# Kernel optimization log

Hardware: AMD Instinct MI355X
Metric: run time of the kernel (lower is better)

The kernel has to match this reference:

```python
import jax, jax.numpy as jnp
import numpy as np
import math

HEAD_DIM = 128
THETA = 10000.0
MASK_VAL = -10000.0


def _rope(x, cos, sin):
    # x: (B, S, D); cos/sin: (S, D//2). Pairs (even, odd) rotated as complex.
    xr = x.reshape(*x.shape[:-1], -1, 2)
    xe, xo = xr[..., 0], xr[..., 1]
    oe = xe * cos - xo * sin
    oo = xe * sin + xo * cos
    return jnp.stack([oe, oo], axis=-1).reshape(x.shape)


def setup_inputs() -> dict:
    key = jax.random.key(0)
    B, S, D = 8, 4096, HEAD_DIM
    qkv = jax.random.normal(key, (B, S, 3 * D), dtype=jnp.float32)
    return {"qkv": qkv}


def reference(qkv):
    B, S, threeD = qkv.shape
    D = threeD // 3
    qkv = qkv.reshape(B, S, 3, D)
    q, k, v = qkv[:, :, 0], qkv[:, :, 1], qkv[:, :, 2]

    # precompute_freqs_cis: outer(t, 1/theta^(2i/d)) -> cos/sin (S, D//2)
    inv_freq = 1.0 / (THETA ** (jnp.arange(0, D, 2, dtype=jnp.float32) / D))
    freqs = jnp.arange(S, dtype=jnp.float32)[:, None] * inv_freq[None, :]
    cos, sin = jnp.cos(freqs), jnp.sin(freqs)
    q = _rope(q, cos, sin)
    k = _rope(k, cos, sin)

    scale = 1.0 / math.sqrt(D)
    scores = jnp.einsum('btd,bsd->bts', q, k) * scale  # (B, S, S)
    causal_mask = jnp.triu(jnp.full((S, S), MASK_VAL, dtype=scores.dtype), 1)
    attn = jax.nn.softmax(scores + causal_mask, axis=-1)
    out = jnp.einsum('bts,bsd->btd', attn, v)  # (B, S, D)
    return out
```

## Files before the change

### kernel.cpp

```cpp
#include <hip/hip_runtime.h>
#include <math.h>

typedef _Float16 half8 __attribute__((ext_vector_type(8)));
typedef float floatx4 __attribute__((ext_vector_type(4)));
typedef float floatx2 __attribute__((ext_vector_type(2)));

#define B_ 8
#define S_ 4096
#define SCALE_L2E 0.12751743008389106f
#define MASK_L2E  -14426.950408889634f
#define L2_10K_OVER_128 0.10381025296522975f

#define PLD2 40
#define KW  136
#define VW  24
#define OSTLD 136
#define SLOTS_PER_B 576
#define NW 8
#define KVBUF 8192
#define NBUF 3
#define POFF (NBUF * KVBUF)
#define POOL_HALFS (POFF + NW * 2 * 16 * PLD2)

__device__ __forceinline__ int chunk_prefix(int qt32) {
    int g = qt32 >> 4;
    return qt32 + 8 * g * (g - 1) + (qt32 - (g << 4)) * g;
}

__device__ __forceinline__ void glds16(const _Float16* src, _Float16* dst) {
    __builtin_amdgcn_global_load_lds((const __attribute__((address_space(1))) void*)src,
                                     (__attribute__((address_space(3))) void*)dst, 16, 0, 0);
}

__global__ __launch_bounds__(256) void prep_kernel(const float* __restrict__ qkv,
                                                   _Float16* __restrict__ Qh,
                                                   _Float16* __restrict__ Kp,
                                                   _Float16* __restrict__ Vp) {
    __shared__ __align__(16) _Float16 Kl[16][KW];
    __shared__ __align__(16) _Float16 Vt[128][VW];
    const int tid = threadIdx.x;
    const int b   = blockIdx.y;
    const int s0  = blockIdx.x * 16;

#pragma unroll
    for (int it = 0; it < 4; ++it) {
        int idx = tid + it * 256;
        int i = idx & 63, sr = idx >> 6, s = s0 + sr;
        const float* base = qkv + ((size_t)(b * S_ + s)) * 384 + 2 * i;
        floatx2 q2 = *(const floatx2*)base;
        floatx2 k2 = *(const floatx2*)(base + 128);
        float inv = exp2f(-(float)(2 * i) * L2_10K_OVER_128);
        float ang = (float)s * inv;
        float sn, cs;
        __sincosf(ang, &sn, &cs);
        size_t oq = ((size_t)(b * S_ + s)) * 128 + 2 * i;
        Qh[oq]     = (_Float16)((q2[0] * cs - q2[1] * sn) * SCALE_L2E);
        Qh[oq + 1] = (_Float16)((q2[0] * sn + q2[1] * cs) * SCALE_L2E);
        Kl[sr][2 * i]     = (_Float16)(k2[0] * cs - k2[1] * sn);
        Kl[sr][2 * i + 1] = (_Float16)(k2[0] * sn + k2[1] * cs);
    }
#pragma unroll
    for (int it = 0; it < 2; ++it) {
        int idx = tid + it * 256;
        int c = idx & 31, sr = idx >> 5;
        floatx4 v = *(const floatx4*)(qkv + ((size_t)(b * S_ + s0 + sr)) * 384 + 256 + c * 4);
#pragma unroll
        for (int j = 0; j < 4; ++j) Vt[c * 4 + j][sr] = (_Float16)v[j];
    }
    __syncthreads();

    {
        int c = tid >> 6, lane = tid & 63;
        int quad = lane >> 4, n = lane & 15;
        half8 val = *(const half8*)&Kl[n][c * 32 + quad * 8];
        int s16 = s0 >> 4;
        *(half8*)(Kp + (((size_t)(b * 256 + s16) * 4 + c) * 64 + lane) * 8) = val;
    }
    {
        int kt = s0 >> 6, c2 = (s0 >> 5) & 1, qp = (s0 >> 4) & 1;
        int nt = tid >> 5, lq = (tid >> 4) & 1, n = tid & 15;
        int quad = qp * 2 + lq;
        int lane = quad * 16 + n;
        half8 val = *(const half8*)&Vt[nt * 16 + n][lq * 8];
        *(half8*)(Vp + ((((size_t)(b * 64 + kt) * 2 + c2) * 8 + nt) * 64 + lane) * 8) = val;
    }
}

__global__ __launch_bounds__(512) void attn_part_kernel(const _Float16* __restrict__ Qh,
                                                        const _Float16* __restrict__ Kp,
                                                        const _Float16* __restrict__ Vp,
                                                        _Float16* __restrict__ Ppart,
                                                        float* __restrict__ Lpart) {
    __shared__ __align__(16) _Float16 POOL[POOL_HALFS];

    const int tid  = threadIdx.x;
    const int w    = tid >> 6;
    const int lane = tid & 63;
    const int quad = lane >> 4;
    const int l16  = lane & 15;
    const int b     = blockIdx.x & 7;
    const int chunk = blockIdx.x >> 3;
    const int c0    = chunk * 8;

    const int qt32_top  = 127 - blockIdx.y * 8;
    const int ktmax_blk = (qt32_top * 32 + 31) >> 6;
    if (c0 > ktmax_blk) return;
    const int kend_blk  = min(ktmax_blk, c0 + 7);

    const int qt32   = qt32_top - w;
    const int qr0    = qt32 * 32;
    const int kt_max = (qr0 + 31) >> 6;
    const bool has_work = (c0 <= kt_max);
    const int kend   = min(kt_max, c0 + 7);
    const int slot   = b * SLOTS_PER_B + chunk_prefix(qt32) + chunk;
    _Float16* Pw = POOL + POFF + w * (2 * 16 * PLD2);

    half8 aq[2][4];
#pragma unroll
    for (int tile = 0; tile < 2; ++tile) {
        const _Float16* Qb = Qh + ((size_t)(b * S_) + qr0 + tile * 16 + l16) * 128;
#pragma unroll
        for (int c = 0; c < 4; ++c) aq[tile][c] = *(const half8*)(Qb + c * 32 + quad * 8);
    }

    floatx4 o[2][8];
#pragma unroll
    for (int tile = 0; tile < 2; ++tile)
#pragma unroll
        for (int i = 0; i < 8; ++i) o[tile][i] = (floatx4){0.f, 0.f, 0.f, 0.f};
    float rsum[2][4] = {{0.f, 0.f, 0.f, 0.f}, {0.f, 0.f, 0.f, 0.f}};

    const _Float16* Kb = Kp + (size_t)b * 524288;
    const _Float16* Vb = Vp + (size_t)b * 524288;

    const int ht0    = 2 * c0;
    const int ht_end = 2 * kend_blk + 1;

#define STAGE(ht_)                                                                \
    do {                                                                          \
        const _Float16* ks_ = Kb + (size_t)(ht_) * 4096 + w * 512 + lane * 8;     \
        const _Float16* vs_ = Vb + (size_t)(ht_) * 4096 + w * 512 + lane * 8;     \
        _Float16* d_ = POOL + ((ht_) % NBUF) * KVBUF + w * 512;                   \
        glds16(ks_, d_);                                                          \
        glds16(vs_, d_ + 4096);                                                   \
    } while (0)

    STAGE(ht0);
    STAGE(ht0 + 1);

    for (int ht = ht0; ht <= ht_end; ++ht) {
        if (ht < ht_end) {
            asm volatile("s_waitcnt vmcnt(2)" ::: "memory");
        } else {
            asm volatile("s_waitcnt vmcnt(0)" ::: "memory");
        }
        __builtin_amdgcn_s_barrier();
        if (ht + 2 <= ht_end) STAGE(ht + 2);

        const int kt = ht >> 1, h = ht & 1;
        if (has_work && kt <= kend) {
            const _Float16* Klds = POOL + (ht % NBUF) * KVBUF;
            const _Float16* Vlds = Klds + 4096;

            floatx4 s4[2][2];
#pragma unroll
            for (int tl = 0; tl < 2; ++tl) {
                half8 bk[4];
#pragma unroll
                for (int c = 0; c < 4; ++c)
                    bk[c] = *(const half8*)&Klds[((tl * 4 + c) * 64 + lane) * 8];
                floatx4 a0 = (floatx4){0.f, 0.f, 0.f, 0.f};
                floatx4 a1 = (floatx4){0.f, 0.f, 0.f, 0.f};
#pragma unroll
                for (int c = 0; c < 4; ++c) {
                    a0 = __builtin_amdgcn_mfma_f32_16x16x32_f16(aq[0][c], bk[c], a0, 0, 0, 0);
                    a1 = __builtin_amdgcn_mfma_f32_16x16x32_f16(aq[1][c], bk[c], a1, 0, 0, 0);
                }
                s4[0][tl] = a0; s4[1][tl] = a1;
            }

            half8 vf[8];
#pragma unroll
            for (int nt = 0; nt < 8; ++nt)
                vf[nt] = *(const half8*)&Vlds[(nt * 64 + lane) * 8];

            if (kt == kt_max) {
#pragma unroll
                for (int tile = 0; tile < 2; ++tile)
#pragma unroll
                    for (int tl = 0; tl < 2; ++tl)
#pragma unroll
                        for (int r = 0; r < 4; ++r) {
                            int kcol = kt * 64 + h * 32 + tl * 16 + l16;
                            int qr   = qr0 + tile * 16 + quad * 4 + r;
                            if (kcol > qr) s4[tile][tl][r] += MASK_L2E;
                        }
            }

#pragma unroll
            for (int tile = 0; tile < 2; ++tile)
#pragma unroll
                for (int tl = 0; tl < 2; ++tl)
#pragma unroll
                    for (int r = 0; r < 4; ++r) {
                        float p = __builtin_amdgcn_exp2f(s4[tile][tl][r]);
                        rsum[tile][r] += p;
                        Pw[tile * (16 * PLD2) + (quad * 4 + r) * PLD2 + tl * 16 + l16] = (_Float16)p;
                    }

#pragma unroll
            for (int tile = 0; tile < 2; ++tile) {
                half8 ap = *(const half8*)&Pw[tile * (16 * PLD2) + l16 * PLD2 + quad * 8];
#pragma unroll
                for (int nt = 0; nt < 8; ++nt)
                    o[tile][nt] = __builtin_amdgcn_mfma_f32_16x16x32_f16(ap, vf[nt], o[tile][nt], 0, 0, 0);
            }
        }
    }
#undef STAGE

    __builtin_amdgcn_s_barrier();

    if (!has_work) return;

#pragma unroll
    for (int off = 1; off <= 8; off <<= 1)
#pragma unroll
        for (int tile = 0; tile < 2; ++tile)
#pragma unroll
            for (int r = 0; r < 4; ++r)
                rsum[tile][r] += __shfl_xor(rsum[tile][r], off, 64);
    if (l16 == 0) {
#pragma unroll
        for (int tile = 0; tile < 2; ++tile)
#pragma unroll
            for (int r = 0; r < 4; ++r)
                Lpart[(size_t)slot * 32 + tile * 16 + quad * 4 + r] = rsum[tile][r];
    }

    _Float16* Ost = POOL + w * (POOL_HALFS / NW);
    _Float16* pp = Ppart + (size_t)slot * 4096;
#pragma unroll
    for (int tile = 0; tile < 2; ++tile) {
#pragma unroll
        for (int nt = 0; nt < 8; ++nt)
#pragma unroll
            for (int r = 0; r < 4; ++r)
                Ost[(quad * 4 + r) * OSTLD + nt * 16 + l16] = (_Float16)o[tile][nt][r];
#pragma unroll
        for (int i = 0; i < 4; ++i) {
            int idx = lane + i * 64;
            half8 v = *(const half8*)&Ost[(idx >> 4) * OSTLD + (idx & 15) * 8];
            *(half8*)(pp + ((size_t)tile * 256 + idx) * 8) = v;
        }
    }
}

__global__ __launch_bounds__(256) void reduce_kernel(const _Float16* __restrict__ Ppart,
                                                     const float* __restrict__ Lpart,
                                                     float* __restrict__ out) {
    const int bid  = blockIdx.x;
    const int b    = bid >> 7;
    const int qt32 = bid & 127;
    const int qr0  = qt32 * 32;
    const int nch  = (((qr0 + 31) >> 6) >> 3) + 1;
    const int slot0 = b * SLOTS_PER_B + chunk_prefix(qt32);
    const _Float16* pp = Ppart + (size_t)slot0 * 4096;
    const float* lp = Lpart + (size_t)slot0 * 32;
    const int tid = threadIdx.x;

#pragma unroll
    for (int j = 0; j < 2; ++j) {
        int idx = tid + j * 256;
        int row = idx >> 4;
        float acc[8] = {0.f, 0.f, 0.f, 0.f, 0.f, 0.f, 0.f, 0.f};
        float l = 0.f;
        for (int c = 0; c < nch; ++c) {
            half8 v = *(const half8*)(pp + (size_t)c * 4096 + (size_t)idx * 8);
#pragma unroll
            for (int k = 0; k < 8; ++k) acc[k] += (float)v[k];
            l += lp[c * 32 + row];
        }
        float inv = 1.0f / l;
        float* ob = out + ((size_t)(b * S_) + qr0) * 128 + (size_t)idx * 8;
        floatx4 o0 = (floatx4){acc[0] * inv, acc[1] * inv, acc[2] * inv, acc[3] * inv};
        floatx4 o1 = (floatx4){acc[4] * inv, acc[5] * inv, acc[6] * inv, acc[7] * inv};
        *(floatx4*)ob = o0;
        *(floatx4*)(ob + 4) = o1;
    }
}

#define PLD 72
__global__ __launch_bounds__(64) void attn_atomic_kernel(const _Float16* __restrict__ Qh,
                                                         const _Float16* __restrict__ Kp,
                                                         const _Float16* __restrict__ Vp,
                                                         float* __restrict__ out,
                                                         float* __restrict__ Lg) {
    __shared__ __align__(16) _Float16 Pl[2][16 * PLD];
    const int lane = threadIdx.x, quad = lane >> 4, l16 = lane & 15;
    const int b = blockIdx.x & 7, chunk = blockIdx.x >> 3;
    const int qt = 255 - blockIdx.y, qr0 = qt * 16;
    const int kt_max = qt >> 2, c0 = chunk * 8;
    if (c0 > kt_max) return;
    const int kend = min(kt_max, c0 + 7);
    const _Float16* Qb = Qh + ((size_t)(b * S_) + qr0 + l16) * 128;
    half8 aq[4];
#pragma unroll
    for (int c = 0; c < 4; ++c) aq[c] = *(const half8*)(Qb + c * 32 + quad * 8);
    floatx4 o[8];
#pragma unroll
    for (int i = 0; i < 8; ++i) o[i] = (floatx4){0.f, 0.f, 0.f, 0.f};
    float rsum[4] = {0.f, 0.f, 0.f, 0.f};
    const _Float16* Kb = Kp + (size_t)b * 524288;
    const _Float16* Vb = Vp + (size_t)b * 524288;
    for (int kt = c0; kt <= kend; ++kt) {
        half8 vf[2][8];
#pragma unroll
        for (int c2 = 0; c2 < 2; ++c2)
#pragma unroll
            for (int nt = 0; nt < 8; ++nt)
                vf[c2][nt] = *(const half8*)(Vb + (((size_t)(kt * 2 + c2) * 8 + nt) * 64 + lane) * 8);
        floatx4 s4[4];
#pragma unroll
        for (int t = 0; t < 4; ++t) {
            const _Float16* kp = Kb + ((size_t)((kt * 4 + t) * 4) * 64 + lane) * 8;
            floatx4 acc = (floatx4){0.f, 0.f, 0.f, 0.f};
#pragma unroll
            for (int c = 0; c < 4; ++c) {
                half8 bk = *(const half8*)(kp + c * 512);
                acc = __builtin_amdgcn_mfma_f32_16x16x32_f16(aq[c], bk, acc, 0, 0, 0);
            }
            s4[t] = acc;
        }
        if (kt == kt_max) {
#pragma unroll
            for (int t = 0; t < 4; ++t)
#pragma unroll
                for (int r = 0; r < 4; ++r) {
                    int kcol = kt * 64 + t * 16 + l16;
                    int qr = qr0 + quad * 4 + r;
                    if (kcol > qr) s4[t][r] += MASK_L2E;
                }
        }
        const int buf = kt & 1;
#pragma unroll
        for (int t = 0; t < 4; ++t)
#pragma unroll
            for (int r = 0; r < 4; ++r) {
                float p = __builtin_amdgcn_exp2f(s4[t][r]);
                rsum[r] += p;
                Pl[buf][(quad * 4 + r) * PLD + t * 16 + l16] = (_Float16)p;
            }
#pragma unroll
        for (int c2 = 0; c2 < 2; ++c2) {
            half8 ap = *(const half8*)&Pl[buf][l16 * PLD + c2 * 32 + quad * 8];
#pragma unroll
            for (int nt = 0; nt < 8; ++nt)
                o[nt] = __builtin_amdgcn_mfma_f32_16x16x32_f16(ap, vf[c2][nt], o[nt], 0, 0, 0);
        }
    }
#pragma unroll
    for (int off = 1; off <= 8; off <<= 1)
#pragma unroll
        for (int r = 0; r < 4; ++r)
            rsum[r] += __shfl_xor(rsum[r], off, 64);
    if (l16 == 0) {
#pragma unroll
        for (int r = 0; r < 4; ++r)
            atomicAdd(&Lg[(size_t)(b * S_) + qr0 + quad * 4 + r], rsum[r]);
    }
    float* ob = out + ((size_t)(b * S_) + qr0) * 128;
#pragma unroll
    for (int nt = 0; nt < 8; ++nt)
#pragma unroll
        for (int r = 0; r < 4; ++r)
            atomicAdd(&ob[(quad * 4 + r) * 128 + nt * 16 + l16], o[nt][r]);
}

__global__ __launch_bounds__(256) void norm_kernel(float* __restrict__ out,
                                                   const float* __restrict__ Lg) {
    int i = blockIdx.x * 256 + threadIdx.x;
    int row = i >> 5;
    floatx4 v = *(floatx4*)(out + (size_t)i * 4);
    float inv = 1.0f / Lg[row];
    v[0] *= inv; v[1] *= inv; v[2] *= inv; v[3] *= inv;
    *(floatx4*)(out + (size_t)i * 4) = v;
}

extern "C" void kernel_launch(void* const* d_in, const int* in_sizes, int n_in,
                              void* d_out, int out_size, void* d_ws, size_t ws_size,
                              hipStream_t stream) {
    const float* qkv = (const float*)d_in[0];
    float* out = (float*)d_out;
    const size_t MB = 1024 * 1024;
    _Float16* Qh = (_Float16*)d_ws;
    _Float16* Kp = (_Float16*)((char*)d_ws + 8 * MB);
    _Float16* Vp = (_Float16*)((char*)d_ws + 16 * MB);

    const size_t lpart_bytes = (size_t)B_ * SLOTS_PER_B * 32 * sizeof(float);
    const size_t ppart_bytes = (size_t)B_ * SLOTS_PER_B * 4096 * sizeof(_Float16);
    const size_t need = 25 * MB + ppart_bytes;

    prep_kernel<<<dim3(256, B_), dim3(256), 0, stream>>>(qkv, Qh, Kp, Vp);

    if (ws_size >= need) {
        float*    Lpart = (float*)((char*)d_ws + 24 * MB);
        _Float16* Ppart = (_Float16*)((char*)d_ws + 25 * MB);
        (void)lpart_bytes;
        attn_part_kernel<<<dim3(64, 16), dim3(512), 0, stream>>>(Qh, Kp, Vp, Ppart, Lpart);
        reduce_kernel<<<dim3(1024), dim3(256), 0, stream>>>(Ppart, Lpart, out);
    } else {
        float* Lg = (float*)((char*)d_ws + 24 * MB);
        hipMemsetAsync(out, 0, (size_t)B_ * S_ * 128 * sizeof(float), stream);
        hipMemsetAsync(Lg, 0, (size_t)B_ * S_ * sizeof(float), stream);
        attn_atomic_kernel<<<dim3(64, 256), dim3(64), 0, stream>>>(Qh, Kp, Vp, out, Lg);
        norm_kernel<<<dim3(4096), dim3(256), 0, stream>>>(out, Lg);
    }
}
```

Baseline: 165.0 us.

## Compute transposed scores so P stays in registers via lane shuffles, drop LDS P staging

The QK^T MFMA operands are swapped so each lane holds scores for one query row across four key columns. The exponentiated probabilities are then packed to fp16 and rearranged with cross-lane shuffles into the A-operand layout for the PV MFMA, which removes the per-wave LDS round trip for P and the extra LDS space. Row sums become one scalar per tile and need fewer shuffles at the end. The grid dimensions are also swapped, which changes the order in which blocks are dispatched.

```diff
diff --git a/kernel.cpp b/kernel.cpp
--- a/kernel.cpp
+++ b/kernel.cpp
@@ -11,7 +11,6 @@
 #define MASK_L2E  -14426.950408889634f
 #define L2_10K_OVER_128 0.10381025296522975f
 
-#define PLD2 40
 #define KW  136
 #define VW  24
 #define OSTLD 136
@@ -19,8 +18,7 @@
 #define NW 8
 #define KVBUF 8192
 #define NBUF 3
-#define POFF (NBUF * KVBUF)
-#define POOL_HALFS (POFF + NW * 2 * 16 * PLD2)
+#define POOL_HALFS (NBUF * KVBUF)
 
 __device__ __forceinline__ int chunk_prefix(int qt32) {
     int g = qt32 >> 4;
@@ -30,6 +28,12 @@
 __device__ __forceinline__ void glds16(const _Float16* src, _Float16* dst) {
     __builtin_amdgcn_global_load_lds((const __attribute__((address_space(1))) void*)src,
                                      (__attribute__((address_space(3))) void*)dst, 16, 0, 0);
+}
+
+__device__ __forceinline__ unsigned pack2(float a, float b) {
+    union { _Float16 h[2]; unsigned u; } x;
+    x.h[0] = (_Float16)a; x.h[1] = (_Float16)b;
+    return x.u;
 }
 
 __global__ __launch_bounds__(256) void prep_kernel(const float* __restrict__ qkv,
@@ -98,11 +102,11 @@
     const int lane = tid & 63;
     const int quad = lane >> 4;
     const int l16  = lane & 15;
-    const int b     = blockIdx.x & 7;
-    const int chunk = blockIdx.x >> 3;
+    const int b     = blockIdx.y & 7;
+    const int chunk = blockIdx.y >> 3;
     const int c0    = chunk * 8;
 
-    const int qt32_top  = 127 - blockIdx.y * 8;
+    const int qt32_top  = 127 - blockIdx.x * 8;
     const int ktmax_blk = (qt32_top * 32 + 31) >> 6;
     if (c0 > ktmax_blk) return;
     const int kend_blk  = min(ktmax_blk, c0 + 7);
@@ -113,7 +117,6 @@
     const bool has_work = (c0 <= kt_max);
     const int kend   = min(kt_max, c0 + 7);
     const int slot   = b * SLOTS_PER_B + chunk_prefix(qt32) + chunk;
-    _Float16* Pw = POOL + POFF + w * (2 * 16 * PLD2);
 
     half8 aq[2][4];
 #pragma unroll
@@ -128,7 +131,7 @@
     for (int tile = 0; tile < 2; ++tile)
 #pragma unroll
         for (int i = 0; i < 8; ++i) o[tile][i] = (floatx4){0.f, 0.f, 0.f, 0.f};
-    float rsum[2][4] = {{0.f, 0.f, 0.f, 0.f}, {0.f, 0.f, 0.f, 0.f}};
+    float rsum[2] = {0.f, 0.f};
 
     const _Float16* Kb = Kp + (size_t)b * 524288;
     const _Float16* Vb = Vp + (size_t)b * 524288;
@@ -162,21 +165,21 @@
             const _Float16* Klds = POOL + (ht % NBUF) * KVBUF;
             const _Float16* Vlds = Klds + 4096;
 
-            floatx4 s4[2][2];
-#pragma unroll
-            for (int tl = 0; tl < 2; ++tl) {
+            floatx4 st[2][2];
+#pragma unroll
+            for (int t = 0; t < 2; ++t) {
                 half8 bk[4];
 #pragma unroll
                 for (int c = 0; c < 4; ++c)
-                    bk[c] = *(const half8*)&Klds[((tl * 4 + c) * 64 + lane) * 8];
+                    bk[c] = *(const half8*)&Klds[((t * 4 + c) * 64 + lane) * 8];
                 floatx4 a0 = (floatx4){0.f, 0.f, 0.f, 0.f};
                 floatx4 a1 = (floatx4){0.f, 0.f, 0.f, 0.f};
 #pragma unroll
                 for (int c = 0; c < 4; ++c) {
-                    a0 = __builtin_amdgcn_mfma_f32_16x16x32_f16(aq[0][c], bk[c], a0, 0, 0, 0);
-                    a1 = __builtin_amdgcn_mfma_f32_16x16x32_f16(aq[1][c], bk[c], a1, 0, 0, 0);
+                    a0 = __builtin_amdgcn_mfma_f32_16x16x32_f16(bk[c], aq[0][c], a0, 0, 0, 0);
+                    a1 = __builtin_amdgcn_mfma_f32_16x16x32_f16(bk[c], aq[1][c], a1, 0, 0, 0);
                 }
-                s4[0][tl] = a0; s4[1][tl] = a1;
+                st[0][t] = a0; st[1][t] = a1;
             }
 
             half8 vf[8];
@@ -188,32 +191,47 @@
 #pragma unroll
                 for (int tile = 0; tile < 2; ++tile)
 #pragma unroll
-                    for (int tl = 0; tl < 2; ++tl)
+                    for (int t = 0; t < 2; ++t)
 #pragma unroll
                         for (int r = 0; r < 4; ++r) {
-                            int kcol = kt * 64 + h * 32 + tl * 16 + l16;
-                            int qr   = qr0 + tile * 16 + quad * 4 + r;
-                            if (kcol > qr) s4[tile][tl][r] += MASK_L2E;
+                            int kcol = kt * 64 + h * 32 + t * 16 + quad * 4 + r;
+                            int qr   = qr0 + tile * 16 + l16;
+                            if (kcol > qr) st[tile][t][r] += MASK_L2E;
                         }
             }
 
 #pragma unroll
-            for (int tile = 0; tile < 2; ++tile)
-#pragma unroll
-                for (int tl = 0; tl < 2; ++tl)
-#pragma unroll
-                    for (int r = 0; r < 4; ++r) {
-                        float p = __builtin_amdgcn_exp2f(s4[tile][tl][r]);
-                        rsum[tile][r] += p;
-                        Pw[tile * (16 * PLD2) + (quad * 4 + r) * PLD2 + tl * 16 + l16] = (_Float16)p;
-                    }
-
-#pragma unroll
             for (int tile = 0; tile < 2; ++tile) {
-                half8 ap = *(const half8*)&Pw[tile * (16 * PLD2) + l16 * PLD2 + quad * 8];
+                float e00 = __builtin_amdgcn_exp2f(st[tile][0][0]);
+                float e01 = __builtin_amdgcn_exp2f(st[tile][0][1]);
+                float e02 = __builtin_amdgcn_exp2f(st[tile][0][2]);
+                float e03 = __builtin_amdgcn_exp2f(st[tile][0][3]);
+                float e10 = __builtin_amdgcn_exp2f(st[tile][1][0]);
+                float e11 = __builtin_amdgcn_exp2f(st[tile][1][1]);
+                float e12 = __builtin_amdgcn_exp2f(st[tile][1][2]);
+                float e13 = __builtin_amdgcn_exp2f(st[tile][1][3]);
+                rsum[tile] += ((e00 + e01) + (e02 + e03)) + ((e10 + e11) + (e12 + e13));
+                unsigned p0a = pack2(e00, e01), p0b = pack2(e02, e03);
+                unsigned p1a = pack2(e10, e11), p1b = pack2(e12, e13);
+                const int base = ((quad & 1) << 5) + l16;
+                unsigned q0a = (unsigned)__shfl((int)p0a, base);
+                unsigned q0b = (unsigned)__shfl((int)p0b, base);
+                unsigned q0c = (unsigned)__shfl((int)p0a, base + 16);
+                unsigned q0d = (unsigned)__shfl((int)p0b, base + 16);
+                unsigned q1a = (unsigned)__shfl((int)p1a, base);
+                unsigned q1b = (unsigned)__shfl((int)p1b, base);
+                unsigned q1c = (unsigned)__shfl((int)p1a, base + 16);
+                unsigned q1d = (unsigned)__shfl((int)p1b, base + 16);
+                const bool hi = (quad & 2) != 0;
+                union { unsigned u[4]; half8 v; } pk;
+                pk.u[0] = hi ? q1a : q0a;
+                pk.u[1] = hi ? q1b : q0b;
+                pk.u[2] = hi ? q1c : q0c;
+                pk.u[3] = hi ? q1d : q0d;
+                half8 pa = pk.v;
 #pragma unroll
                 for (int nt = 0; nt < 8; ++nt)
-                    o[tile][nt] = __builtin_amdgcn_mfma_f32_16x16x32_f16(ap, vf[nt], o[tile][nt], 0, 0, 0);
+                    o[tile][nt] = __builtin_amdgcn_mfma_f32_16x16x32_f16(pa, vf[nt], o[tile][nt], 0, 0, 0);
             }
         }
     }
@@ -224,18 +242,14 @@
     if (!has_work) return;
 
 #pragma unroll
-    for (int off = 1; off <= 8; off <<= 1)
+    for (int tile = 0; tile < 2; ++tile) {
+        rsum[tile] += __shfl_xor(rsum[tile], 16, 64);
+        rsum[tile] += __shfl_xor(rsum[tile], 32, 64);
+    }
+    if (quad == 0) {
 #pragma unroll
         for (int tile = 0; tile < 2; ++tile)
-#pragma unroll
-            for (int r = 0; r < 4; ++r)
-                rsum[tile][r] += __shfl_xor(rsum[tile][r], off, 64);
-    if (l16 == 0) {
-#pragma unroll
-        for (int tile = 0; tile < 2; ++tile)
-#pragma unroll
-            for (int r = 0; r < 4; ++r)
-                Lpart[(size_t)slot * 32 + tile * 16 + quad * 4 + r] = rsum[tile][r];
+            Lpart[(size_t)slot * 32 + tile * 16 + l16] = rsum[tile];
     }
 
     _Float16* Ost = POOL + w * (POOL_HALFS / NW);
@@ -407,7 +421,7 @@
         float*    Lpart = (float*)((char*)d_ws + 24 * MB);
         _Float16* Ppart = (_Float16*)((char*)d_ws + 25 * MB);
         (void)lpart_bytes;
-        attn_part_kernel<<<dim3(64, 16), dim3(512), 0, stream>>>(Qh, Kp, Vp, Ppart, Lpart);
+        attn_part_kernel<<<dim3(16, 64), dim3(512), 0, stream>>>(Qh, Kp, Vp, Ppart, Lpart);
         reduce_kernel<<<dim3(1024), dim3(256), 0, stream>>>(Ppart, Lpart, out);
     } else {
         float* Lg = (float*)((char*)d_ws + 24 * MB);
```

Measured after the change: 183.7 us. +11.3%, slower.

## Give each wave 64 query rows and compact the split-K grid to active blocks

Applied to the files above, without the earlier changes.

Each wave now owns a 64-row query tile (four 16-row MFMA tiles) instead of 32 rows, and each block has 4 waves instead of 8. Every K/V fragment loaded from LDS is therefore reused across twice as many query rows. The grid enumerates only blocks that have work instead of launching blocks that exit early. The costs are much higher register pressure from 4x8 accumulators, fewer waves per block for latency hiding, and a different partial-buffer layout in the reduction.

```diff
diff --git a/kernel.cpp b/kernel.cpp
--- a/kernel.cpp
+++ b/kernel.cpp
@@ -15,16 +15,16 @@
 #define KW  136
 #define VW  24
 #define OSTLD 136
-#define SLOTS_PER_B 576
-#define NW 8
+#define SLOTS64_PER_B 288
+#define NW 4
 #define KVBUF 8192
 #define NBUF 3
 #define POFF (NBUF * KVBUF)
-#define POOL_HALFS (POFF + NW * 2 * 16 * PLD2)
-
-__device__ __forceinline__ int chunk_prefix(int qt32) {
-    int g = qt32 >> 4;
-    return qt32 + 8 * g * (g - 1) + (qt32 - (g << 4)) * g;
+#define POOL_HALFS (POFF + NW * 16 * PLD2)
+
+__device__ __forceinline__ int chunk_prefix64(int i) {
+    int g = i >> 3;
+    return i + 4 * g * (g - 1) + (i - (g << 3)) * g;
 }
 
 __device__ __forceinline__ void glds16(const _Float16* src, _Float16* dst) {
@@ -86,7 +86,7 @@
     }
 }
 
-__global__ __launch_bounds__(512) void attn_part_kernel(const _Float16* __restrict__ Qh,
+__global__ __launch_bounds__(256) void attn_part_kernel(const _Float16* __restrict__ Qh,
                                                         const _Float16* __restrict__ Kp,
                                                         const _Float16* __restrict__ Vp,
                                                         _Float16* __restrict__ Ppart,
@@ -98,37 +98,41 @@
     const int lane = tid & 63;
     const int quad = lane >> 4;
     const int l16  = lane & 15;
-    const int b     = blockIdx.x & 7;
-    const int chunk = blockIdx.x >> 3;
+    const int b    = blockIdx.x;
+
+    int u = blockIdx.y, g = 0;
+    for (;;) { int c = ((63 - 4 * g) >> 3) + 1; if (u < c) break; u -= c; ++g; }
+    const int chunk = u;
     const int c0    = chunk * 8;
-
-    const int qt32_top  = 127 - blockIdx.y * 8;
-    const int ktmax_blk = (qt32_top * 32 + 31) >> 6;
-    if (c0 > ktmax_blk) return;
-    const int kend_blk  = min(ktmax_blk, c0 + 7);
-
-    const int qt32   = qt32_top - w;
-    const int qr0    = qt32 * 32;
-    const int kt_max = (qr0 + 31) >> 6;
+    const int i_top = 63 - 4 * g;
+    const int kend_blk = min(i_top, c0 + 7);
+
+    const int unit  = i_top - w;
+    const int qr0   = unit * 64;
+    const int kt_max = unit;
     const bool has_work = (c0 <= kt_max);
-    const int kend   = min(kt_max, c0 + 7);
-    const int slot   = b * SLOTS_PER_B + chunk_prefix(qt32) + chunk;
-    _Float16* Pw = POOL + POFF + w * (2 * 16 * PLD2);
-
-    half8 aq[2][4];
-#pragma unroll
-    for (int tile = 0; tile < 2; ++tile) {
+    const int kend  = min(kt_max, c0 + 7);
+    const int slot  = b * SLOTS64_PER_B + chunk_prefix64(unit) + chunk;
+    _Float16* Pw = POOL + POFF + w * (16 * PLD2);
+
+    half8 aq[4][4];
+#pragma unroll
+    for (int tile = 0; tile < 4; ++tile) {
         const _Float16* Qb = Qh + ((size_t)(b * S_) + qr0 + tile * 16 + l16) * 128;
 #pragma unroll
         for (int c = 0; c < 4; ++c) aq[tile][c] = *(const half8*)(Qb + c * 32 + quad * 8);
     }
 
-    floatx4 o[2][8];
-#pragma unroll
-    for (int tile = 0; tile < 2; ++tile)
+    floatx4 o[4][8];
+#pragma unroll
+    for (int tile = 0; tile < 4; ++tile)
 #pragma unroll
         for (int i = 0; i < 8; ++i) o[tile][i] = (floatx4){0.f, 0.f, 0.f, 0.f};
-    float rsum[2][4] = {{0.f, 0.f, 0.f, 0.f}, {0.f, 0.f, 0.f, 0.f}};
+    float rsum[4][4];
+#pragma unroll
+    for (int tile = 0; tile < 4; ++tile)
+#pragma unroll
+        for (int r = 0; r < 4; ++r) rsum[tile][r] = 0.f;
 
     const _Float16* Kb = Kp + (size_t)b * 524288;
     const _Float16* Vb = Vp + (size_t)b * 524288;
@@ -138,11 +142,13 @@
 
 #define STAGE(ht_)                                                                \
     do {                                                                          \
-        const _Float16* ks_ = Kb + (size_t)(ht_) * 4096 + w * 512 + lane * 8;     \
-        const _Float16* vs_ = Vb + (size_t)(ht_) * 4096 + w * 512 + lane * 8;     \
-        _Float16* d_ = POOL + ((ht_) % NBUF) * KVBUF + w * 512;                   \
+        const _Float16* ks_ = Kb + (size_t)(ht_) * 4096 + w * 1024 + lane * 8;    \
+        const _Float16* vs_ = Vb + (size_t)(ht_) * 4096 + w * 1024 + lane * 8;    \
+        _Float16* d_ = POOL + ((ht_) % NBUF) * KVBUF + w * 1024;                  \
         glds16(ks_, d_);                                                          \
+        glds16(ks_ + 512, d_ + 512);                                              \
         glds16(vs_, d_ + 4096);                                                   \
+        glds16(vs_ + 512, d_ + 4096 + 512);                                       \
     } while (0)
 
     STAGE(ht0);
@@ -150,7 +156,7 @@
 
     for (int ht = ht0; ht <= ht_end; ++ht) {
         if (ht < ht_end) {
-            asm volatile("s_waitcnt vmcnt(2)" ::: "memory");
+            asm volatile("s_waitcnt vmcnt(4)" ::: "memory");
         } else {
             asm volatile("s_waitcnt vmcnt(0)" ::: "memory");
         }
@@ -162,55 +168,44 @@
             const _Float16* Klds = POOL + (ht % NBUF) * KVBUF;
             const _Float16* Vlds = Klds + 4096;
 
-            floatx4 s4[2][2];
-#pragma unroll
-            for (int tl = 0; tl < 2; ++tl) {
-                half8 bk[4];
+            half8 bk[2][4];
+#pragma unroll
+            for (int tl = 0; tl < 2; ++tl)
 #pragma unroll
                 for (int c = 0; c < 4; ++c)
-                    bk[c] = *(const half8*)&Klds[((tl * 4 + c) * 64 + lane) * 8];
-                floatx4 a0 = (floatx4){0.f, 0.f, 0.f, 0.f};
-                floatx4 a1 = (floatx4){0.f, 0.f, 0.f, 0.f};
-#pragma unroll
-                for (int c = 0; c < 4; ++c) {
-                    a0 = __builtin_amdgcn_mfma_f32_16x16x32_f16(aq[0][c], bk[c], a0, 0, 0, 0);
-                    a1 = __builtin_amdgcn_mfma_f32_16x16x32_f16(aq[1][c], bk[c], a1, 0, 0, 0);
-                }
-                s4[0][tl] = a0; s4[1][tl] = a1;
-            }
-
+                    bk[tl][c] = *(const half8*)&Klds[((tl * 4 + c) * 64 + lane) * 8];
             half8 vf[8];
 #pragma unroll
             for (int nt = 0; nt < 8; ++nt)
                 vf[nt] = *(const half8*)&Vlds[(nt * 64 + lane) * 8];
 
-            if (kt == kt_max) {
-#pragma unroll
-                for (int tile = 0; tile < 2; ++tile)
-#pragma unroll
-                    for (int tl = 0; tl < 2; ++tl)
-#pragma unroll
-                        for (int r = 0; r < 4; ++r) {
-                            int kcol = kt * 64 + h * 32 + tl * 16 + l16;
-                            int qr   = qr0 + tile * 16 + quad * 4 + r;
-                            if (kcol > qr) s4[tile][tl][r] += MASK_L2E;
-                        }
-            }
-
-#pragma unroll
-            for (int tile = 0; tile < 2; ++tile)
-#pragma unroll
-                for (int tl = 0; tl < 2; ++tl)
+#pragma unroll
+            for (int tile = 0; tile < 4; ++tile) {
+                floatx4 s0 = (floatx4){0.f, 0.f, 0.f, 0.f};
+                floatx4 s1 = (floatx4){0.f, 0.f, 0.f, 0.f};
+#pragma unroll
+                for (int c = 0; c < 4; ++c) {
+                    s0 = __builtin_amdgcn_mfma_f32_16x16x32_f16(aq[tile][c], bk[0][c], s0, 0, 0, 0);
+                    s1 = __builtin_amdgcn_mfma_f32_16x16x32_f16(aq[tile][c], bk[1][c], s1, 0, 0, 0);
+                }
+                if (kt == kt_max) {
 #pragma unroll
                     for (int r = 0; r < 4; ++r) {
-                        float p = __builtin_amdgcn_exp2f(s4[tile][tl][r]);
-                        rsum[tile][r] += p;
-                        Pw[tile * (16 * PLD2) + (quad * 4 + r) * PLD2 + tl * 16 + l16] = (_Float16)p;
+                        int qr = qr0 + tile * 16 + quad * 4 + r;
+                        int k0 = kt * 64 + h * 32 + l16;
+                        if (k0 > qr)      s0[r] += MASK_L2E;
+                        if (k0 + 16 > qr) s1[r] += MASK_L2E;
                     }
-
-#pragma unroll
-            for (int tile = 0; tile < 2; ++tile) {
-                half8 ap = *(const half8*)&Pw[tile * (16 * PLD2) + l16 * PLD2 + quad * 8];
+                }
+#pragma unroll
+                for (int r = 0; r < 4; ++r) {
+                    float p0 = __builtin_amdgcn_exp2f(s0[r]);
+                    float p1 = __builtin_amdgcn_exp2f(s1[r]);
+                    rsum[tile][r] += p0 + p1;
+                    Pw[(quad * 4 + r) * PLD2 + l16]      = (_Float16)p0;
+                    Pw[(quad * 4 + r) * PLD2 + 16 + l16] = (_Float16)p1;
+                }
+                half8 ap = *(const half8*)&Pw[l16 * PLD2 + quad * 8];
 #pragma unroll
                 for (int nt = 0; nt < 8; ++nt)
                     o[tile][nt] = __builtin_amdgcn_mfma_f32_16x16x32_f16(ap, vf[nt], o[tile][nt], 0, 0, 0);
@@ -226,22 +221,22 @@
 #pragma unroll
     for (int off = 1; off <= 8; off <<= 1)
 #pragma unroll
-        for (int tile = 0; tile < 2; ++tile)
+        for (int tile = 0; tile < 4; ++tile)
 #pragma unroll
             for (int r = 0; r < 4; ++r)
                 rsum[tile][r] += __shfl_xor(rsum[tile][r], off, 64);
     if (l16 == 0) {
 #pragma unroll
-        for (int tile = 0; tile < 2; ++tile)
+        for (int tile = 0; tile < 4; ++tile)
 #pragma unroll
             for (int r = 0; r < 4; ++r)
-                Lpart[(size_t)slot * 32 + tile * 16 + quad * 4 + r] = rsum[tile][r];
+                Lpart[(size_t)slot * 64 + tile * 16 + quad * 4 + r] = rsum[tile][r];
     }
 
     _Float16* Ost = POOL + w * (POOL_HALFS / NW);
-    _Float16* pp = Ppart + (size_t)slot * 4096;
-#pragma unroll
-    for (int tile = 0; tile < 2; ++tile) {
+    _Float16* pp = Ppart + (size_t)slot * 8192;
+#pragma unroll
+    for (int tile = 0; tile < 4; ++tile) {
 #pragma unroll
         for (int nt = 0; nt < 8; ++nt)
 #pragma unroll
@@ -251,7 +246,7 @@
         for (int i = 0; i < 4; ++i) {
             int idx = lane + i * 64;
             half8 v = *(const half8*)&Ost[(idx >> 4) * OSTLD + (idx & 15) * 8];
-            *(half8*)(pp + ((size_t)tile * 256 + idx) * 8) = v;
+            *(half8*)(pp + ((size_t)tile * 2048 + (size_t)idx * 8)) = v;
         }
     }
 }
@@ -260,26 +255,26 @@
                                                      const float* __restrict__ Lpart,
                                                      float* __restrict__ out) {
     const int bid  = blockIdx.x;
-    const int b    = bid >> 7;
-    const int qt32 = bid & 127;
-    const int qr0  = qt32 * 32;
-    const int nch  = (((qr0 + 31) >> 6) >> 3) + 1;
-    const int slot0 = b * SLOTS_PER_B + chunk_prefix(qt32);
-    const _Float16* pp = Ppart + (size_t)slot0 * 4096;
-    const float* lp = Lpart + (size_t)slot0 * 32;
+    const int b    = bid >> 6;
+    const int unit = bid & 63;
+    const int qr0  = unit * 64;
+    const int nch  = (unit >> 3) + 1;
+    const int slot0 = b * SLOTS64_PER_B + chunk_prefix64(unit);
+    const _Float16* pp = Ppart + (size_t)slot0 * 8192;
+    const float* lp = Lpart + (size_t)slot0 * 64;
     const int tid = threadIdx.x;
 
 #pragma unroll
-    for (int j = 0; j < 2; ++j) {
+    for (int j = 0; j < 4; ++j) {
         int idx = tid + j * 256;
         int row = idx >> 4;
         float acc[8] = {0.f, 0.f, 0.f, 0.f, 0.f, 0.f, 0.f, 0.f};
         float l = 0.f;
         for (int c = 0; c < nch; ++c) {
-            half8 v = *(const half8*)(pp + (size_t)c * 4096 + (size_t)idx * 8);
+            half8 v = *(const half8*)(pp + (size_t)c * 8192 + (size_t)idx * 8);
 #pragma unroll
             for (int k = 0; k < 8; ++k) acc[k] += (float)v[k];
-            l += lp[c * 32 + row];
+            l += lp[c * 64 + row];
         }
         float inv = 1.0f / l;
         float* ob = out + ((size_t)(b * S_) + qr0) * 128 + (size_t)idx * 8;
@@ -397,8 +392,8 @@
     _Float16* Kp = (_Float16*)((char*)d_ws + 8 * MB);
     _Float16* Vp = (_Float16*)((char*)d_ws + 16 * MB);
 
-    const size_t lpart_bytes = (size_t)B_ * SLOTS_PER_B * 32 * sizeof(float);
-    const size_t ppart_bytes = (size_t)B_ * SLOTS_PER_B * 4096 * sizeof(_Float16);
+    const size_t lpart_bytes = (size_t)B_ * SLOTS64_PER_B * 64 * sizeof(float);
+    const size_t ppart_bytes = (size_t)B_ * SLOTS64_PER_B * 8192 * sizeof(_Float16);
     const size_t need = 25 * MB + ppart_bytes;
 
     prep_kernel<<<dim3(256, B_), dim3(256), 0, stream>>>(qkv, Qh, Kp, Vp);
@@ -407,8 +402,8 @@
         float*    Lpart = (float*)((char*)d_ws + 24 * MB);
         _Float16* Ppart = (_Float16*)((char*)d_ws + 25 * MB);
         (void)lpart_bytes;
-        attn_part_kernel<<<dim3(64, 16), dim3(512), 0, stream>>>(Qh, Kp, Vp, Ppart, Lpart);
-        reduce_kernel<<<dim3(1024), dim3(256), 0, stream>>>(Ppart, Lpart, out);
+        attn_part_kernel<<<dim3(8, 72), dim3(256), 0, stream>>>(Qh, Kp, Vp, Ppart, Lpart);
+        reduce_kernel<<<dim3(512), dim3(256), 0, stream>>>(Ppart, Lpart, out);
     } else {
         float* Lg = (float*)((char*)d_ws + 24 * MB);
         hipMemsetAsync(out, 0, (size_t)B_ * S_ * 128 * sizeof(float), stream);
```

Result: slower. 208.1 us (+26.1%).

## Fuse split-KV reduction into attention kernel via last-arriver atomic counters

Applied to the files above, without the earlier changes.

Removes the separate reduce kernel. Each attention wave bumps a per-(batch, query-tile) counter after writing its partial output, and the last chunk to arrive sums all partials and writes the normalized result. Counters are zeroed in the prep kernel. This saves a kernel launch and lets the reduction overlap with attention work. The cost is threadfences, atomics and a tail of reduction work done by single waves.

```diff
diff --git a/kernel.cpp b/kernel.cpp
--- a/kernel.cpp
+++ b/kernel.cpp
@@ -35,12 +35,15 @@
 __global__ __launch_bounds__(256) void prep_kernel(const float* __restrict__ qkv,
                                                    _Float16* __restrict__ Qh,
                                                    _Float16* __restrict__ Kp,
-                                                   _Float16* __restrict__ Vp) {
+                                                   _Float16* __restrict__ Vp,
+                                                   int* Cnt) {
     __shared__ __align__(16) _Float16 Kl[16][KW];
     __shared__ __align__(16) _Float16 Vt[128][VW];
     const int tid = threadIdx.x;
     const int b   = blockIdx.y;
     const int s0  = blockIdx.x * 16;
+
+    if (Cnt && blockIdx.y == 0 && blockIdx.x < 4) Cnt[blockIdx.x * 256 + tid] = 0;
 
 #pragma unroll
     for (int it = 0; it < 4; ++it) {
@@ -90,7 +93,9 @@
                                                         const _Float16* __restrict__ Kp,
                                                         const _Float16* __restrict__ Vp,
                                                         _Float16* __restrict__ Ppart,
-                                                        float* __restrict__ Lpart) {
+                                                        float* __restrict__ Lpart,
+                                                        int* __restrict__ Cnt,
+                                                        float* __restrict__ out) {
     __shared__ __align__(16) _Float16 POOL[POOL_HALFS];
 
     const int tid  = threadIdx.x;
@@ -254,39 +259,35 @@
             *(half8*)(pp + ((size_t)tile * 256 + idx) * 8) = v;
         }
     }
-}
-
-__global__ __launch_bounds__(256) void reduce_kernel(const _Float16* __restrict__ Ppart,
-                                                     const float* __restrict__ Lpart,
-                                                     float* __restrict__ out) {
-    const int bid  = blockIdx.x;
-    const int b    = bid >> 7;
-    const int qt32 = bid & 127;
-    const int qr0  = qt32 * 32;
-    const int nch  = (((qr0 + 31) >> 6) >> 3) + 1;
-    const int slot0 = b * SLOTS_PER_B + chunk_prefix(qt32);
-    const _Float16* pp = Ppart + (size_t)slot0 * 4096;
-    const float* lp = Lpart + (size_t)slot0 * 32;
-    const int tid = threadIdx.x;
-
-#pragma unroll
-    for (int j = 0; j < 2; ++j) {
-        int idx = tid + j * 256;
-        int row = idx >> 4;
-        float acc[8] = {0.f, 0.f, 0.f, 0.f, 0.f, 0.f, 0.f, 0.f};
-        float l = 0.f;
-        for (int c = 0; c < nch; ++c) {
-            half8 v = *(const half8*)(pp + (size_t)c * 4096 + (size_t)idx * 8);
-#pragma unroll
-            for (int k = 0; k < 8; ++k) acc[k] += (float)v[k];
-            l += lp[c * 32 + row];
-        }
-        float inv = 1.0f / l;
-        float* ob = out + ((size_t)(b * S_) + qr0) * 128 + (size_t)idx * 8;
-        floatx4 o0 = (floatx4){acc[0] * inv, acc[1] * inv, acc[2] * inv, acc[3] * inv};
-        floatx4 o1 = (floatx4){acc[4] * inv, acc[5] * inv, acc[6] * inv, acc[7] * inv};
-        *(floatx4*)ob = o0;
-        *(floatx4*)(ob + 4) = o1;
+
+    __threadfence();
+    int old = 0;
+    if (lane == 0) old = atomicAdd(&Cnt[b * 128 + qt32], 1);
+    old = __shfl(old, 0, 64);
+    const int nch = (kt_max >> 3) + 1;
+    if (old == nch - 1) {
+        __threadfence();
+        const size_t slot0 = (size_t)(b * SLOTS_PER_B + chunk_prefix(qt32));
+        const _Float16* pr = Ppart + slot0 * 4096;
+        const float*    lr = Lpart + slot0 * 32;
+        float* ob = out + ((size_t)(b * S_) + qr0) * 128;
+#pragma unroll
+        for (int it = 0; it < 8; ++it) {
+            int idx = lane + it * 64;
+            int row = idx >> 4;
+            float acc[8] = {0.f, 0.f, 0.f, 0.f, 0.f, 0.f, 0.f, 0.f};
+            float l = 0.f;
+            for (int c = 0; c < nch; ++c) {
+                half8 v = *(const half8*)(pr + (size_t)c * 4096 + (size_t)idx * 8);
+#pragma unroll
+                for (int k = 0; k < 8; ++k) acc[k] += (float)v[k];
+                l += lr[c * 32 + row];
+            }
+            float inv = 1.0f / l;
+            float* op = ob + (size_t)idx * 8;
+            *(floatx4*)op       = (floatx4){acc[0] * inv, acc[1] * inv, acc[2] * inv, acc[3] * inv};
+            *(floatx4*)(op + 4) = (floatx4){acc[4] * inv, acc[5] * inv, acc[6] * inv, acc[7] * inv};
+        }
     }
 }
 
@@ -393,23 +394,22 @@
     const float* qkv = (const float*)d_in[0];
     float* out = (float*)d_out;
     const size_t MB = 1024 * 1024;
+    const size_t KB = 1024;
     _Float16* Qh = (_Float16*)d_ws;
     _Float16* Kp = (_Float16*)((char*)d_ws + 8 * MB);
     _Float16* Vp = (_Float16*)((char*)d_ws + 16 * MB);
 
-    const size_t lpart_bytes = (size_t)B_ * SLOTS_PER_B * 32 * sizeof(float);
     const size_t ppart_bytes = (size_t)B_ * SLOTS_PER_B * 4096 * sizeof(_Float16);
     const size_t need = 25 * MB + ppart_bytes;
 
-    prep_kernel<<<dim3(256, B_), dim3(256), 0, stream>>>(qkv, Qh, Kp, Vp);
-
     if (ws_size >= need) {
         float*    Lpart = (float*)((char*)d_ws + 24 * MB);
+        int*      Cnt   = (int*)((char*)d_ws + 24 * MB + 640 * KB);
         _Float16* Ppart = (_Float16*)((char*)d_ws + 25 * MB);
-        (void)lpart_bytes;
-        attn_part_kernel<<<dim3(64, 16), dim3(512), 0, stream>>>(Qh, Kp, Vp, Ppart, Lpart);
-        reduce_kernel<<<dim3(1024), dim3(256), 0, stream>>>(Ppart, Lpart, out);
+        prep_kernel<<<dim3(256, B_), dim3(256), 0, stream>>>(qkv, Qh, Kp, Vp, Cnt);
+        attn_part_kernel<<<dim3(64, 16), dim3(512), 0, stream>>>(Qh, Kp, Vp, Ppart, Lpart, Cnt, out);
     } else {
+        prep_kernel<<<dim3(256, B_), dim3(256), 0, stream>>>(qkv, Qh, Kp, Vp, nullptr);
         float* Lg = (float*)((char*)d_ws + 24 * MB);
         hipMemsetAsync(out, 0, (size_t)B_ * S_ * 128 * sizeof(float), stream);
         hipMemsetAsync(Lg, 0, (size_t)B_ * S_ * sizeof(float), stream);
```

Measured after the change: 325.9 us. 97.5% more time.
